# Kernel optimization log

Measured on AMD Instinct MI355X. Metric: run time of the kernel, lower is better.

## Reference

```python
import jax, jax.numpy as jnp
import numpy as np
from jax import lax

RSM_K = 35
PFM_K = 31


def _box_sum(x, k):
    # Separable zero-padded box sum, equivalent to conv2d with a uniform kxk
    # kernel and padding=k//2 (odd k -> SAME). x: [B,1,H,W]
    p = k // 2
    pad = ((0, 0), (0, 0), (p, p), (0, 0))
    x = lax.reduce_window(x, 0.0, lax.add, (1, 1, k, 1), (1, 1, 1, 1), pad)
    pad = ((0, 0), (0, 0), (0, 0), (p, p))
    x = lax.reduce_window(x, 0.0, lax.add, (1, 1, 1, k), (1, 1, 1, 1), pad)
    return x


def _dilate(x, k):
    # Separable morphological dilation == max_pool2d(kernel=k, stride=1, pad=k//2).
    # -inf padding matches torch's max_pool2d padding semantics for 0/1 masks.
    p = k // 2
    ninf = -jnp.inf
    pad = ((0, 0), (0, 0), (p, p), (0, 0))
    x = lax.reduce_window(x, ninf, lax.max, (1, 1, k, 1), (1, 1, 1, 1), pad)
    pad = ((0, 0), (0, 0), (0, 0), (p, p))
    x = lax.reduce_window(x, ninf, lax.max, (1, 1, 1, k), (1, 1, 1, 1), pad)
    return x


def setup_inputs() -> dict:
    key = jax.random.key(0)
    # Sparse binary lesion mask, values exactly 0.0 / 1.0, shape [B,1,H,W]
    masks = (jax.random.uniform(key, (32, 1, 768, 768)) < 0.02).astype(jnp.float32)
    return {"masks": masks}


def reference(masks):
    # RSM: probability map = uniform 35x35 box average (conv2d with 1/k^2 kernel)
    rsm = _box_sum(masks, RSM_K) * (1.0 / (RSM_K * RSM_K))  # [B,1,H,W]
    # PFM: 1 = lesion, 0 = surrounding (inside 31x31 dilation), 2 = ignore
    dilated = _dilate(masks, PFM_K)
    pfm = jnp.where(masks > 0.5, 1, jnp.where(dilated > 0.5, 0, 2))
    pfm = pfm.astype(jnp.int32)[:, 0, :, :]  # [B,H,W]
    return rsm, pfm
```

## Files before the change

### kernel.cpp

```cpp
#include <hip/hip_runtime.h>


#define BATCH 32
#define HH 768
#define WW 768
#define NPIX (HH * WW)

constexpr int TYO  = 48;
constexpr int HALO = 17;
constexpr int ROWS = TYO + 2 * HALO;
constexpr int NSEG = 12;
constexpr int SSEG = NSEG + 2;

__global__ __launch_bounds__(256)
void label_gen_fused(const float* __restrict__ in, float* __restrict__ out) {
    __shared__ unsigned long long sbits[ROWS][SSEG];

    const int tid  = threadIdx.x;
    const int lane = tid & 63;
    const int wv   = tid >> 6;
    const int y0   = blockIdx.x * TYO;
    const int b    = blockIdx.y;
    const float* __restrict__ src = in + (size_t)b * NPIX;

    for (int lr = wv; lr < ROWS; lr += 4) {
        const int r = y0 - HALO + lr;
        unsigned long long bb[NSEG];
        if ((unsigned)r < (unsigned)HH) {
            const float* rp = src + (size_t)r * WW;
            #pragma unroll
            for (int j = 0; j < NSEG; ++j)
                bb[j] = __ballot(rp[64 * j + lane] > 0.5f);
        } else {
            #pragma unroll
            for (int j = 0; j < NSEG; ++j) bb[j] = 0ull;
        }
        if (lane == 0) {
            sbits[lr][0] = 0ull;
            #pragma unroll
            for (int j = 0; j < NSEG; ++j) sbits[lr][j + 1] = bb[j];
            sbits[lr][SSEG - 1] = 0ull;
        }
    }
    __syncthreads();

    if (tid >= 192) return;
    const int c0 = 4 * tid;
    const int s  = c0 - HALO;
    const int q  = (s >> 6) + 1;
    const int sh = s & 63;

    auto win = [&](int lr) -> unsigned long long {
        const unsigned long long lo = sbits[lr][q];
        const unsigned long long hi = sbits[lr][q + 1];
        return (lo >> sh) | (hi << (64 - sh));
    };
    const unsigned long long M35 = (1ull << 35) - 1;
    const unsigned long long M31 = (1ull << 31) - 1;
    auto h35swar = [&](unsigned long long w) -> uint2 {
        const int h0 = (int)__popcll(w & M35);
        const int h1 = h0 + (int)((w >> 35) & 1) - (int)(w & 1);
        const int h2 = h1 + (int)((w >> 36) & 1) - (int)((w >> 1) & 1);
        const int h3 = h2 + (int)((w >> 37) & 1) - (int)((w >> 2) & 1);
        return make_uint2((unsigned)(h0 | (h1 << 16)), (unsigned)(h2 | (h3 << 16)));
    };
    auto h31swar = [&](unsigned long long w) -> uint2 {
        const int h0 = (int)__popcll((w >> 2) & M31);
        const int h1 = h0 + (int)((w >> 33) & 1) - (int)((w >> 2) & 1);
        const int h2 = h1 + (int)((w >> 34) & 1) - (int)((w >> 3) & 1);
        const int h3 = h2 + (int)((w >> 35) & 1) - (int)((w >> 4) & 1);
        return make_uint2((unsigned)(h0 | (h1 << 16)), (unsigned)(h2 | (h3 << 16)));
    };

    uint2 v35 = make_uint2(0u, 0u), v31 = make_uint2(0u, 0u);
    #pragma unroll
    for (int k = 0; k < 35; ++k) {
        const unsigned long long w = win(k);
        const uint2 a = h35swar(w);
        v35.x += a.x; v35.y += a.y;
        if (k >= 2 && k <= 32) {
            const uint2 d = h31swar(w);
            v31.x += d.x; v31.y += d.y;
        }
    }

    const int mq = (c0 >> 6) + 1;
    const int mb = c0 & 63;
    float* orow = out + (size_t)b * NPIX + (size_t)y0 * WW + c0;
    float* prow = orow + (size_t)BATCH * NPIX;

    for (int i = 0; i < TYO; ++i) {
        const int lr = i + HALO;
        const unsigned long long mword = sbits[lr][mq];

        float4 r4, p4;
        r4.x = (float)(v35.x & 0xFFFFu) * (1.0f / 1225.0f);
        r4.y = (float)(v35.x >> 16)     * (1.0f / 1225.0f);
        r4.z = (float)(v35.y & 0xFFFFu) * (1.0f / 1225.0f);
        r4.w = (float)(v35.y >> 16)     * (1.0f / 1225.0f);
        {
            const int m0 = (int)((mword >> mb) & 1ull);
            const int m1 = (int)((mword >> (mb + 1)) & 1ull);
            const int m2 = (int)((mword >> (mb + 2)) & 1ull);
            const int m3 = (int)((mword >> (mb + 3)) & 1ull);
            p4.x = m0 ? 1.0f : ((v31.x & 0xFFFFu) ? 0.0f : 2.0f);
            p4.y = m1 ? 1.0f : ((v31.x >> 16)     ? 0.0f : 2.0f);
            p4.z = m2 ? 1.0f : ((v31.y & 0xFFFFu) ? 0.0f : 2.0f);
            p4.w = m3 ? 1.0f : ((v31.y >> 16)     ? 0.0f : 2.0f);
        }
        *(float4*)orow = r4;
        *(float4*)prow = p4;
        orow += WW; prow += WW;

        if (i < TYO - 1) {
            const uint2 e35 = h35swar(win(lr + 18));
            const uint2 l35 = h35swar(win(lr - 17));
            const uint2 e31 = h31swar(win(lr + 16));
            const uint2 l31 = h31swar(win(lr - 15));
            v35.x = v35.x + e35.x - l35.x;  v35.y = v35.y + e35.y - l35.y;
            v31.x = v31.x + e31.x - l31.x;  v31.y = v31.y + e31.y - l31.y;
        }
    }
}

extern "C" void kernel_launch(void* const* d_in, const int* in_sizes, int n_in,
                              void* d_out, int out_size, void* d_ws, size_t ws_size,
                              hipStream_t stream) {
    const float* masks = (const float*)d_in[0];
    float* out = (float*)d_out;
    dim3 grid(HH / TYO, BATCH);
    label_gen_fused<<<grid, 256, 0, stream>>>(masks, out);
}
```

Baseline: 217.6 us.

## Use 512 threads, split rows into four groups, six columns per thread

Doubles the block to 512 threads so the bitmask load uses 8 waves. The compute phase now uses every thread instead of 192: four row groups of 12 output rows each, with 128 threads per group covering 6 columns apiece. The goal is more parallelism and latency hiding in the sliding-window phase. In exchange, each row group recomputes its own 35-row initial window sum, stores become float2 instead of float4, and register use per thread rises.

```diff
diff --git a/kernel.cpp b/kernel.cpp
--- a/kernel.cpp
+++ b/kernel.cpp
@@ -11,8 +11,15 @@
 constexpr int ROWS = TYO + 2 * HALO;
 constexpr int NSEG = 12;
 constexpr int SSEG = NSEG + 2;
+constexpr int NT   = 512;
+constexpr int NG   = 4;
+constexpr int RPG  = TYO / NG;
+constexpr int CT   = 128;
+constexpr int CPT  = 6;
 
-__global__ __launch_bounds__(256)
+struct U3 { unsigned x, y, z; };
+
+__global__ __launch_bounds__(NT)
 void label_gen_fused(const float* __restrict__ in, float* __restrict__ out) {
     __shared__ unsigned long long sbits[ROWS][SSEG];
 
@@ -23,7 +30,7 @@
     const int b    = blockIdx.y;
     const float* __restrict__ src = in + (size_t)b * NPIX;
 
-    for (int lr = wv; lr < ROWS; lr += 4) {
+    for (int lr = wv; lr < ROWS; lr += 8) {
         const int r = y0 - HALO + lr;
         unsigned long long bb[NSEG];
         if ((unsigned)r < (unsigned)HH) {
@@ -44,81 +51,94 @@
     }
     __syncthreads();
 
-    if (tid >= 192) return;
-    const int c0 = 4 * tid;
-    const int s  = c0 - HALO;
-    const int q  = (s >> 6) + 1;
-    const int sh = s & 63;
+    const int g   = tid >> 7;
+    const int ct  = tid & (CT - 1);
+    const int c0  = CPT * ct;
+    const int yb  = y0 + RPG * g;
+    const int lr0 = RPG * g;
+    const int s   = c0 - HALO;
+    const int q   = (s >> 6) + 1;
+    const int sh  = s & 63;
 
     auto win = [&](int lr) -> unsigned long long {
-        const unsigned long long lo = sbits[lr][q];
-        const unsigned long long hi = sbits[lr][q + 1];
-        return (lo >> sh) | (hi << (64 - sh));
+        return (sbits[lr][q] >> sh) | (sbits[lr][q + 1] << (64 - sh));
     };
     const unsigned long long M35 = (1ull << 35) - 1;
     const unsigned long long M31 = (1ull << 31) - 1;
-    auto h35swar = [&](unsigned long long w) -> uint2 {
+    auto bit = [](unsigned long long w, int k) -> int { return (int)((w >> k) & 1ull); };
+
+    auto h35swar = [&](unsigned long long w) -> U3 {
         const int h0 = (int)__popcll(w & M35);
-        const int h1 = h0 + (int)((w >> 35) & 1) - (int)(w & 1);
-        const int h2 = h1 + (int)((w >> 36) & 1) - (int)((w >> 1) & 1);
-        const int h3 = h2 + (int)((w >> 37) & 1) - (int)((w >> 2) & 1);
-        return make_uint2((unsigned)(h0 | (h1 << 16)), (unsigned)(h2 | (h3 << 16)));
+        const int h1 = h0 + bit(w, 35) - bit(w, 0);
+        const int h2 = h1 + bit(w, 36) - bit(w, 1);
+        const int h3 = h2 + bit(w, 37) - bit(w, 2);
+        const int h4 = h3 + bit(w, 38) - bit(w, 3);
+        const int h5 = h4 + bit(w, 39) - bit(w, 4);
+        return U3{(unsigned)(h0 | (h1 << 16)), (unsigned)(h2 | (h3 << 16)),
+                  (unsigned)(h4 | (h5 << 16))};
     };
-    auto h31swar = [&](unsigned long long w) -> uint2 {
-        const int h0 = (int)__popcll((w >> 2) & M31);
-        const int h1 = h0 + (int)((w >> 33) & 1) - (int)((w >> 2) & 1);
-        const int h2 = h1 + (int)((w >> 34) & 1) - (int)((w >> 3) & 1);
-        const int h3 = h2 + (int)((w >> 35) & 1) - (int)((w >> 4) & 1);
-        return make_uint2((unsigned)(h0 | (h1 << 16)), (unsigned)(h2 | (h3 << 16)));
+    auto h31swar = [&](unsigned long long w) -> U3 {
+        const int d0 = (int)__popcll((w >> 2) & M31);
+        const int d1 = d0 + bit(w, 33) - bit(w, 2);
+        const int d2 = d1 + bit(w, 34) - bit(w, 3);
+        const int d3 = d2 + bit(w, 35) - bit(w, 4);
+        const int d4 = d3 + bit(w, 36) - bit(w, 5);
+        const int d5 = d4 + bit(w, 37) - bit(w, 6);
+        return U3{(unsigned)(d0 | (d1 << 16)), (unsigned)(d2 | (d3 << 16)),
+                  (unsigned)(d4 | (d5 << 16))};
     };
 
-    uint2 v35 = make_uint2(0u, 0u), v31 = make_uint2(0u, 0u);
+    U3 v35{0, 0, 0}, v31{0, 0, 0};
     #pragma unroll
     for (int k = 0; k < 35; ++k) {
-        const unsigned long long w = win(k);
-        const uint2 a = h35swar(w);
-        v35.x += a.x; v35.y += a.y;
+        const unsigned long long w = win(lr0 + k);
+        const U3 a = h35swar(w);
+        v35.x += a.x; v35.y += a.y; v35.z += a.z;
         if (k >= 2 && k <= 32) {
-            const uint2 d = h31swar(w);
-            v31.x += d.x; v31.y += d.y;
+            const U3 d = h31swar(w);
+            v31.x += d.x; v31.y += d.y; v31.z += d.z;
         }
     }
 
-    const int mq = (c0 >> 6) + 1;
-    const int mb = c0 & 63;
-    float* orow = out + (size_t)b * NPIX + (size_t)y0 * WW + c0;
+    float* orow = out + (size_t)b * NPIX + (size_t)yb * WW + c0;
     float* prow = orow + (size_t)BATCH * NPIX;
 
-    for (int i = 0; i < TYO; ++i) {
-        const int lr = i + HALO;
-        const unsigned long long mword = sbits[lr][mq];
+    for (int i = 0; i < RPG; ++i) {
+        const int lr = lr0 + HALO + i;
+        const unsigned long long mwin = win(lr);
 
-        float4 r4, p4;
-        r4.x = (float)(v35.x & 0xFFFFu) * (1.0f / 1225.0f);
-        r4.y = (float)(v35.x >> 16)     * (1.0f / 1225.0f);
-        r4.z = (float)(v35.y & 0xFFFFu) * (1.0f / 1225.0f);
-        r4.w = (float)(v35.y >> 16)     * (1.0f / 1225.0f);
-        {
-            const int m0 = (int)((mword >> mb) & 1ull);
-            const int m1 = (int)((mword >> (mb + 1)) & 1ull);
-            const int m2 = (int)((mword >> (mb + 2)) & 1ull);
-            const int m3 = (int)((mword >> (mb + 3)) & 1ull);
-            p4.x = m0 ? 1.0f : ((v31.x & 0xFFFFu) ? 0.0f : 2.0f);
-            p4.y = m1 ? 1.0f : ((v31.x >> 16)     ? 0.0f : 2.0f);
-            p4.z = m2 ? 1.0f : ((v31.y & 0xFFFFu) ? 0.0f : 2.0f);
-            p4.w = m3 ? 1.0f : ((v31.y >> 16)     ? 0.0f : 2.0f);
-        }
-        *(float4*)orow = r4;
-        *(float4*)prow = p4;
+        const float2 r01 = make_float2((float)(v35.x & 0xFFFFu) * (1.0f / 1225.0f),
+                                       (float)(v35.x >> 16)     * (1.0f / 1225.0f));
+        const float2 r23 = make_float2((float)(v35.y & 0xFFFFu) * (1.0f / 1225.0f),
+                                       (float)(v35.y >> 16)     * (1.0f / 1225.0f));
+        const float2 r45 = make_float2((float)(v35.z & 0xFFFFu) * (1.0f / 1225.0f),
+                                       (float)(v35.z >> 16)     * (1.0f / 1225.0f));
+        auto pv = [&](int k, unsigned dfield) -> float {
+            return bit(mwin, 17 + k) ? 1.0f : (dfield ? 0.0f : 2.0f);
+        };
+        const float2 p01 = make_float2(pv(0, v31.x & 0xFFFFu), pv(1, v31.x >> 16));
+        const float2 p23 = make_float2(pv(2, v31.y & 0xFFFFu), pv(3, v31.y >> 16));
+        const float2 p45 = make_float2(pv(4, v31.z & 0xFFFFu), pv(5, v31.z >> 16));
+
+        *(float2*)(orow + 0) = r01;
+        *(float2*)(orow + 2) = r23;
+        *(float2*)(orow + 4) = r45;
+        *(float2*)(prow + 0) = p01;
+        *(float2*)(prow + 2) = p23;
+        *(float2*)(prow + 4) = p45;
         orow += WW; prow += WW;
 
-        if (i < TYO - 1) {
-            const uint2 e35 = h35swar(win(lr + 18));
-            const uint2 l35 = h35swar(win(lr - 17));
-            const uint2 e31 = h31swar(win(lr + 16));
-            const uint2 l31 = h31swar(win(lr - 15));
-            v35.x = v35.x + e35.x - l35.x;  v35.y = v35.y + e35.y - l35.y;
-            v31.x = v31.x + e31.x - l31.x;  v31.y = v31.y + e31.y - l31.y;
+        if (i < RPG - 1) {
+            const U3 e35 = h35swar(win(lr + 18));
+            const U3 l35 = h35swar(win(lr - 17));
+            const U3 e31 = h31swar(win(lr + 16));
+            const U3 l31 = h31swar(win(lr - 15));
+            v35.x = v35.x + e35.x - l35.x;
+            v35.y = v35.y + e35.y - l35.y;
+            v35.z = v35.z + e35.z - l35.z;
+            v31.x = v31.x + e31.x - l31.x;
+            v31.y = v31.y + e31.y - l31.y;
+            v31.z = v31.z + e31.z - l31.z;
         }
     }
 }
@@ -129,5 +149,5 @@
     const float* masks = (const float*)d_in[0];
     float* out = (float*)d_out;
     dim3 grid(HH / TYO, BATCH);
-    label_gen_fused<<<grid, 256, 0, stream>>>(masks, out);
+    label_gen_fused<<<grid, NT, 0, stream>>>(masks, out);
 }
```

Result: faster. 213.0 us (-2.1%).

## Split each tile's output rows across four thread groups with 768-thread blocks

Applied to the files above, without the earlier changes.

Blocks grow from 256 to 768 threads. The load phase now uses 12 waves. The compute phase splits the 48 output rows into 4 groups of 12, one per 192-thread group, instead of having 64 threads idle and 192 threads walk all 48 rows serially. This shortens the serial sliding-window chain per thread and uses all threads. In exchange, each group recomputes its own 35-row initial window sum, adding redundant popcount work and raising register pressure.

```diff
diff --git a/kernel.cpp b/kernel.cpp
--- a/kernel.cpp
+++ b/kernel.cpp
@@ -11,8 +11,13 @@
 constexpr int ROWS = TYO + 2 * HALO;
 constexpr int NSEG = 12;
 constexpr int SSEG = NSEG + 2;
+constexpr int NT   = 768;
+constexpr int NG   = 4;
+constexpr int RPG  = TYO / NG;
+constexpr int CT   = 192;
+constexpr int CPT  = 4;
 
-__global__ __launch_bounds__(256)
+__global__ __launch_bounds__(NT)
 void label_gen_fused(const float* __restrict__ in, float* __restrict__ out) {
     __shared__ unsigned long long sbits[ROWS][SSEG];
 
@@ -23,7 +28,7 @@
     const int b    = blockIdx.y;
     const float* __restrict__ src = in + (size_t)b * NPIX;
 
-    for (int lr = wv; lr < ROWS; lr += 4) {
+    for (int lr = wv; lr < ROWS; lr += 12) {
         const int r = y0 - HALO + lr;
         unsigned long long bb[NSEG];
         if ((unsigned)r < (unsigned)HH) {
@@ -44,38 +49,41 @@
     }
     __syncthreads();
 
-    if (tid >= 192) return;
-    const int c0 = 4 * tid;
-    const int s  = c0 - HALO;
-    const int q  = (s >> 6) + 1;
-    const int sh = s & 63;
+    const int g   = tid / CT;
+    const int ct  = tid - g * CT;
+    const int c0  = CPT * ct;
+    const int yb  = y0 + RPG * g;
+    const int lr0 = RPG * g;
+    const int s   = c0 - HALO;
+    const int q   = (s >> 6) + 1;
+    const int sh  = s & 63;
 
     auto win = [&](int lr) -> unsigned long long {
-        const unsigned long long lo = sbits[lr][q];
-        const unsigned long long hi = sbits[lr][q + 1];
-        return (lo >> sh) | (hi << (64 - sh));
+        return (sbits[lr][q] >> sh) | (sbits[lr][q + 1] << (64 - sh));
     };
     const unsigned long long M35 = (1ull << 35) - 1;
     const unsigned long long M31 = (1ull << 31) - 1;
+    auto bit = [](unsigned long long w, int k) -> int { return (int)((w >> k) & 1ull); };
+
     auto h35swar = [&](unsigned long long w) -> uint2 {
         const int h0 = (int)__popcll(w & M35);
-        const int h1 = h0 + (int)((w >> 35) & 1) - (int)(w & 1);
-        const int h2 = h1 + (int)((w >> 36) & 1) - (int)((w >> 1) & 1);
-        const int h3 = h2 + (int)((w >> 37) & 1) - (int)((w >> 2) & 1);
+        const int h1 = h0 + bit(w, 35) - bit(w, 0);
+        const int h2 = h1 + bit(w, 36) - bit(w, 1);
+        const int h3 = h2 + bit(w, 37) - bit(w, 2);
         return make_uint2((unsigned)(h0 | (h1 << 16)), (unsigned)(h2 | (h3 << 16)));
     };
     auto h31swar = [&](unsigned long long w) -> uint2 {
-        const int h0 = (int)__popcll((w >> 2) & M31);
-        const int h1 = h0 + (int)((w >> 33) & 1) - (int)((w >> 2) & 1);
-        const int h2 = h1 + (int)((w >> 34) & 1) - (int)((w >> 3) & 1);
-        const int h3 = h2 + (int)((w >> 35) & 1) - (int)((w >> 4) & 1);
-        return make_uint2((unsigned)(h0 | (h1 << 16)), (unsigned)(h2 | (h3 << 16)));
+        const int d0 = (int)__popcll((w >> 2) & M31);
+        const int d1 = d0 + bit(w, 33) - bit(w, 2);
+        const int d2 = d1 + bit(w, 34) - bit(w, 3);
+        const int d3 = d2 + bit(w, 35) - bit(w, 4);
+        return make_uint2((unsigned)(d0 | (d1 << 16)), (unsigned)(d2 | (d3 << 16)));
     };
 
     uint2 v35 = make_uint2(0u, 0u), v31 = make_uint2(0u, 0u);
     #pragma unroll
     for (int k = 0; k < 35; ++k) {
-        const unsigned long long w = win(k);
+        const unsigned long long w = win(lr0 + k);
         const uint2 a = h35swar(w);
         v35.x += a.x; v35.y += a.y;
         if (k >= 2 && k <= 32) {
@@ -84,35 +92,28 @@
         }
     }
 
-    const int mq = (c0 >> 6) + 1;
-    const int mb = c0 & 63;
-    float* orow = out + (size_t)b * NPIX + (size_t)y0 * WW + c0;
+    float* orow = out + (size_t)b * NPIX + (size_t)yb * WW + c0;
     float* prow = orow + (size_t)BATCH * NPIX;
 
-    for (int i = 0; i < TYO; ++i) {
-        const int lr = i + HALO;
-        const unsigned long long mword = sbits[lr][mq];
+    for (int i = 0; i < RPG; ++i) {
+        const int lr = lr0 + HALO + i;
+        const unsigned long long mwin = win(lr);
 
         float4 r4, p4;
         r4.x = (float)(v35.x & 0xFFFFu) * (1.0f / 1225.0f);
         r4.y = (float)(v35.x >> 16)     * (1.0f / 1225.0f);
         r4.z = (float)(v35.y & 0xFFFFu) * (1.0f / 1225.0f);
         r4.w = (float)(v35.y >> 16)     * (1.0f / 1225.0f);
-        {
-            const int m0 = (int)((mword >> mb) & 1ull);
-            const int m1 = (int)((mword >> (mb + 1)) & 1ull);
-            const int m2 = (int)((mword >> (mb + 2)) & 1ull);
-            const int m3 = (int)((mword >> (mb + 3)) & 1ull);
-            p4.x = m0 ? 1.0f : ((v31.x & 0xFFFFu) ? 0.0f : 2.0f);
-            p4.y = m1 ? 1.0f : ((v31.x >> 16)     ? 0.0f : 2.0f);
-            p4.z = m2 ? 1.0f : ((v31.y & 0xFFFFu) ? 0.0f : 2.0f);
-            p4.w = m3 ? 1.0f : ((v31.y >> 16)     ? 0.0f : 2.0f);
-        }
+        p4.x = bit(mwin, 17) ? 1.0f : ((v31.x & 0xFFFFu) ? 0.0f : 2.0f);
+        p4.y = bit(mwin, 18) ? 1.0f : ((v31.x >> 16)     ? 0.0f : 2.0f);
+        p4.z = bit(mwin, 19) ? 1.0f : ((v31.y & 0xFFFFu) ? 0.0f : 2.0f);
+        p4.w = bit(mwin, 20) ? 1.0f : ((v31.y >> 16)     ? 0.0f : 2.0f);
+
         *(float4*)orow = r4;
         *(float4*)prow = p4;
         orow += WW; prow += WW;
 
-        if (i < TYO - 1) {
+        if (i < RPG - 1) {
             const uint2 e35 = h35swar(win(lr + 18));
             const uint2 l35 = h35swar(win(lr - 17));
             const uint2 e31 = h31swar(win(lr + 16));
@@ -129,5 +130,5 @@
     const float* masks = (const float*)d_in[0];
     float* out = (float*)d_out;
     dim3 grid(HH / TYO, BATCH);
-    label_gen_fused<<<grid, 256, 0, stream>>>(masks, out);
+    label_gen_fused<<<grid, NT, 0, stream>>>(masks, out);
 }
```

Measured after the change: 213.9 us. About the same (-1.7%).
